# Optimization experiments

Hardware: AMD Instinct MI355X
Metric: run time of the kernel (lower is better)

Reference implementation:

```python
import jax, jax.numpy as jnp
import numpy as np


def _lstm_layer(x, Wih, Whh, b):
    # torch nn.LSTM single layer, batch_first, gates in i,f,g,o order
    B, T, _ = x.shape
    H = Whh.shape[1]
    xg = jnp.einsum('btd,gd->btg', x, Wih) + b  # precompute input gates (B,T,4H)

    def step(carry, g_t):
        h, c = carry
        g = g_t + h @ Whh.T
        i, f, gg, o = jnp.split(g, 4, axis=-1)
        c = jax.nn.sigmoid(f) * c + jax.nn.sigmoid(i) * jnp.tanh(gg)
        h = jax.nn.sigmoid(o) * jnp.tanh(c)
        return (h, c), h

    z = jnp.zeros((B, H), x.dtype)
    _, hs = jax.lax.scan(step, (z, z), jnp.swapaxes(xg, 0, 1))
    return jnp.swapaxes(hs, 0, 1)


def _forward(x, x_lens, word_starts, word_ends, word_lens, tail_frames,
             fW_ih0, fW_hh0, fb0, fW_ih1, fW_hh1, fb1, fW_ih2, fW_hh2, fb2,
             fpW, fpb, wpW, wpb, lnW, lnB, wW_ih, wW_hh, wb, spW, spb):
    B, T, _ = x.shape
    # 3-layer frame LSTM (eval mode: inter-layer dropout disabled)
    h = _lstm_layer(x, fW_ih0, fW_hh0, fb0)
    h = _lstm_layer(h, fW_ih1, fW_hh1, fb1)
    h = _lstm_layer(h, fW_ih2, fW_hh2, fb2)
    # pad_packed_sequence zeros outputs beyond each sequence length
    tmask = (jnp.arange(T)[None, :] < x_lens[:, None]).astype(h.dtype)
    h = h * tmask[..., None]
    y_frame = h @ fpW.T + fpb  # (B,T,srv)

    # ragged per-word tail mean: r_j = mean h[i0:ef], i0 = max(ef-tail, sf)
    W = word_ends.shape[1]
    ef = jnp.minimum(word_ends, x_lens[:, None])
    sf = jnp.maximum(word_starts, 0)
    i0 = jnp.maximum(ef - tail_frames, sf)
    valid = ((jnp.arange(W)[None, :] < word_lens[:, None]) & (word_ends > 0)
             & (ef > sf) & (ef > i0))
    t = jnp.arange(T)
    m = (valid[:, :, None] & (t[None, None, :] >= i0[:, :, None])
         & (t[None, None, :] < ef[:, :, None])).astype(h.dtype)  # (B,W,T)
    cnt = jnp.maximum(m.sum(-1), 1.0)
    reps = jnp.einsum('bwt,bth->bwh', m, h) / cnt[..., None]  # (B,W,FH)

    # word_proj: Linear + LayerNorm + GELU (eval: dropout/noise/word-dropout off)
    r = reps @ wpW.T + wpb
    mu = r.mean(-1, keepdims=True)
    var = ((r - mu) ** 2).mean(-1, keepdims=True)
    r = (r - mu) / jnp.sqrt(var + 1e-5) * lnW + lnB
    r = jax.nn.gelu(r, approximate=False)

    lens = jnp.maximum(word_lens, 1)
    c = _lstm_layer(r, wW_ih, wW_hh, wb)
    wmask = (jnp.arange(W)[None, :] < lens[:, None]).astype(c.dtype)
    c = c * wmask[..., None]  # pad_packed(total_length=W) zeros
    pred_sem = c @ spW.T + spb  # (B,W,srv)
    return y_frame, x_lens, pred_sem


def setup_inputs() -> dict:
    key = jax.random.key(0)
    ks = jax.random.split(key, 24)
    B, T, D, SRV, FH, WR, WH, W = 16, 2000, 80, 512, 512, 256, 256, 100
    x = jax.random.normal(ks[0], (B, T, D), jnp.float32)
    x_lens = jax.random.randint(ks[1], (B,), T // 2, T + 1).at[0].set(T)
    ends = jnp.sort(jax.random.randint(ks[2], (B, W), 1, T + 1), axis=1)
    starts = jnp.concatenate([jnp.zeros((B, 1), ends.dtype), ends[:, :-1]], axis=1)
    word_lens = jax.random.randint(ks[3], (B,), 1, W + 1)

    def u(k, shape, fan):
        s = 1.0 / np.sqrt(fan)
        return jax.random.uniform(k, shape, jnp.float32, -s, s)

    return {
        'x': x, 'x_lens': x_lens, 'word_starts': starts, 'word_ends': ends,
        'word_lens': word_lens, 'tail_frames': 10,
        'fW_ih0': u(ks[4], (4 * FH, D), FH), 'fW_hh0': u(ks[5], (4 * FH, FH), FH), 'fb0': u(ks[6], (4 * FH,), FH),
        'fW_ih1': u(ks[7], (4 * FH, FH), FH), 'fW_hh1': u(ks[8], (4 * FH, FH), FH), 'fb1': u(ks[9], (4 * FH,), FH),
        'fW_ih2': u(ks[10], (4 * FH, FH), FH), 'fW_hh2': u(ks[11], (4 * FH, FH), FH), 'fb2': u(ks[12], (4 * FH,), FH),
        'fpW': u(ks[13], (SRV, FH), FH), 'fpb': u(ks[14], (SRV,), FH),
        'wpW': u(ks[15], (WR, FH), FH), 'wpb': u(ks[16], (WR,), FH),
        'lnW': jnp.ones((WR,), jnp.float32), 'lnB': jnp.zeros((WR,), jnp.float32),
        'wW_ih': u(ks[17], (4 * WH, WR), WH), 'wW_hh': u(ks[18], (4 * WH, WH), WH), 'wb': u(ks[19], (4 * WH,), WH),
        'spW': u(ks[20], (SRV, WH), WH), 'spb': u(ks[21], (SRV,), WH),
    }


def reference(x, x_lens, word_starts, word_ends, word_lens, tail_frames,
              fW_ih0, fW_hh0, fb0, fW_ih1, fW_hh1, fb1, fW_ih2, fW_hh2, fb2,
              fpW, fpb, wpW, wpb, lnW, lnB, wW_ih, wW_hh, wb, spW, spb):
    return _forward(x, x_lens, word_starts, word_ends, word_lens, tail_frames,
                    fW_ih0, fW_hh0, fb0, fW_ih1, fW_hh1, fb1, fW_ih2, fW_hh2, fb2,
                    fpW, fpb, wpW, wpb, lnW, lnB, wW_ih, wW_hh, wb, spW, spb)
```

## Files before the change

kernel.cpp:

```cpp
#include <hip/hip_runtime.h>
#include <math.h>

typedef unsigned short u16;
typedef unsigned int   u32;
typedef unsigned long long u64;
typedef __attribute__((ext_vector_type(8))) short short8;
typedef __attribute__((ext_vector_type(4))) float f32x4;

__device__ __forceinline__ float bf2f(u16 v) { return __uint_as_float(((u32)v) << 16); }
__device__ __forceinline__ u16 f2bf(float f) {
    u32 u = __float_as_uint(f);
    u32 r = (u + 0x7fffu + ((u >> 16) & 1u)) >> 16;
    return (u16)r;
}
__device__ __forceinline__ u32 pk2(float a, float b) {
    return ((u32)f2bf(a)) | (((u32)f2bf(b)) << 16);
}
__device__ __forceinline__ float sigm(float x) { return 1.f / (1.f + __expf(-x)); }
__device__ __forceinline__ f32x4 mfma16(short8 a, short8 b, f32x4 c) {
    return __builtin_amdgcn_mfma_f32_16x16x32_bf16(a, b, c, 0, 0, 0);
}
__device__ __forceinline__ short8 ld8bf(const float* p) {
    short8 r;
#pragma unroll
    for (int j = 0; j < 8; ++j) r[j] = (short)f2bf(p[j]);
    return r;
}
__device__ __forceinline__ short8 ldg16cv(const u16* p) {
    short8 r;
    asm volatile("global_load_dwordx4 %0, %1, off sc0 sc1" : "=v"(r) : "v"(p));
    return r;
}
__device__ __forceinline__ void waitvm() {
    asm volatile("s_waitcnt vmcnt(0)" ::: "memory");
}

#define FLAG_STRIDE 16
#define NPAR 8
#define BIGF (1 << 26)
#define XL_OFF 16384000
#define PS_OFF 16384016

#define WS_FLAGS   0
#define WS_HBUF_F  32768
#define WS_HBUF_W  425984
#define WS_REPS    491520
#define WS_RW      3768320
#define WS_HSEQ    4587520
#define WS_FPWB    6225920

template<int KTIN, bool L0>
__device__ __forceinline__ void frame_body(
    const int layer, const int kwg,
    const float* __restrict__ Wih, const float* __restrict__ Whh, const float* __restrict__ bias,
    const float* __restrict__ x, u16* __restrict__ hbuf, int* __restrict__ flags,
    float* __restrict__ h3out, float* sC, u16* sxpad, u16* AsIn, u16* AsOwn)
{
    const int tid  = threadIdx.x;
    const int lane = tid & 63;
    const int wave = tid >> 6;
    const int n16  = lane & 15;
    const int quad = lane >> 4;
    const int koff = quad * 8;

    if (L0) {
        for (int e = tid; e < 256; e += 128) sxpad[(e >> 4) * 96 + 80 + (e & 15)] = 0;
    }

    const int grow = wave * 1024 + ((n16 >> 3) * 512) + kwg * 8 + (n16 & 7);
    short8 bfr[KTIN + 16];
#pragma unroll
    for (int kt = 0; kt < KTIN; ++kt) {
        short8 v = {0,0,0,0,0,0,0,0};
        const int k = kt * 32 + koff;
        if (L0) { if (k + 8 <= 80) v = ld8bf(Wih + grow * 80 + k); }
        else    { v = ld8bf(Wih + (size_t)grow * 512 + k); }
        bfr[kt] = v;
    }
#pragma unroll
    for (int kt = 0; kt < 16; ++kt)
        bfr[KTIN + kt] = ld8bf(Whh + (size_t)grow * 512 + kt * 32 + koff);

    const int gb = tid & 15;
    const int gp4 = (tid >> 4) & 3;
    const int c0 = kwg * 8 + gp4 * 2;
    const float bI0 = bias[c0],        bI1 = bias[c0 + 1];
    const float bF0 = bias[512 + c0],  bF1 = bias[512 + c0 + 1];
    const float bG0 = bias[1024 + c0], bG1 = bias[1024 + c0 + 1];
    const float bO0 = bias[1536 + c0], bO1 = bias[1536 + c0 + 1];
    float cp0 = 0.f, cp1 = 0.f;

    const int* fP = flags + (layer * 64) * FLAG_STRIDE;
    const int* fO = flags + ((layer + 1) * 64) * FLAG_STRIDE;
    const int* fN = flags + ((layer + 2) * 64) * FLAG_STRIDE;
    int* myflag   = flags + ((layer + 1) * 64 + kwg) * FLAG_STRIDE;
    __syncthreads();

    for (int t = 0; t < 2000; ++t) {
        if (wave == 0) {
            int guard = 0;
            for (;;) {
                const int fp = __hip_atomic_load(fP + lane * FLAG_STRIDE, __ATOMIC_RELAXED, __HIP_MEMORY_SCOPE_AGENT);
                const int fo = __hip_atomic_load(fO + lane * FLAG_STRIDE, __ATOMIC_RELAXED, __HIP_MEMORY_SCOPE_AGENT);
                const int fn = __hip_atomic_load(fN + lane * FLAG_STRIDE, __ATOMIC_RELAXED, __HIP_MEMORY_SCOPE_AGENT);
                if (__all((fp >= t + 1) && (fo >= t) && (fn >= t - 7))) break;
                if (++guard > (1 << 22)) break;
                __builtin_amdgcn_s_sleep(1);
            }
        }
        __syncthreads();

        const u16* hown = hbuf + ((size_t)(layer * NPAR + ((t + 7) & 7))) * 8192;
        short8 rin[8], rown[8];
        float4 xv0, xv1, xv2;
        if (L0) {
            const int e0 = tid, e1 = tid + 128, e2 = tid + 256;
            xv0 = *(const float4*)(x + ((size_t)(e0 / 20) * 2000 + t) * 80 + (e0 % 20) * 4);
            xv1 = *(const float4*)(x + ((size_t)(e1 / 20) * 2000 + t) * 80 + (e1 % 20) * 4);
            if (e2 < 320)
                xv2 = *(const float4*)(x + ((size_t)(e2 / 20) * 2000 + t) * 80 + (e2 % 20) * 4);
        } else {
            const u16* hin = hbuf + ((size_t)((layer - 1) * NPAR + (t & 7))) * 8192;
#pragma unroll
            for (int i = 0; i < 8; ++i) rin[i] = ldg16cv(hin + (tid + 128 * i) * 8);
        }
#pragma unroll
        for (int i = 0; i < 8; ++i) rown[i] = ldg16cv(hown + (tid + 128 * i) * 8);
        waitvm();
        if (L0) {
            const int e0 = tid, e1 = tid + 128, e2 = tid + 256;
            u32* d0 = (u32*)(sxpad + (e0 / 20) * 96 + (e0 % 20) * 4);
            d0[0] = pk2(xv0.x, xv0.y); d0[1] = pk2(xv0.z, xv0.w);
            u32* d1 = (u32*)(sxpad + (e1 / 20) * 96 + (e1 % 20) * 4);
            d1[0] = pk2(xv1.x, xv1.y); d1[1] = pk2(xv1.z, xv1.w);
            if (e2 < 320) {
                u32* d2 = (u32*)(sxpad + (e2 / 20) * 96 + (e2 % 20) * 4);
                d2[0] = pk2(xv2.x, xv2.y); d2[1] = pk2(xv2.z, xv2.w);
            }
        }
#pragma unroll
        for (int i = 0; i < 8; ++i) {
            const int c = tid + 128 * i;
            const int row = c >> 6, col8 = (c & 63) << 3;
            if (!L0) *(short8*)(AsIn + row * 520 + col8) = rin[i];
            *(short8*)(AsOwn + row * 520 + col8) = rown[i];
        }
        __syncthreads();

        f32x4 acc[4] = {{0,0,0,0},{0,0,0,0},{0,0,0,0},{0,0,0,0}};
#pragma unroll
        for (int kt = 0; kt < KTIN; ++kt) {
            short8 a;
            if (L0) a = *(const short8*)(sxpad + n16 * 96 + kt * 32 + koff);
            else    a = *(const short8*)(AsIn + n16 * 520 + kt * 32 + koff);
            acc[kt & 3] = mfma16(a, bfr[kt], acc[kt & 3]);
        }
#pragma unroll
        for (int kt = 0; kt < 16; ++kt) {
            short8 a = *(const short8*)(AsOwn + n16 * 520 + kt * 32 + koff);
            acc[(KTIN + kt) & 3] = mfma16(a, bfr[KTIN + kt], acc[(KTIN + kt) & 3]);
        }
        const f32x4 C = acc[0] + acc[1] + acc[2] + acc[3];
#pragma unroll
        for (int r = 0; r < 4; ++r)
            sC[(wave * 16 + quad * 4 + r) * 17 + n16] = C[r];
        __syncthreads();

        if (tid < 64) {
            const int b = gb, p = gp4;
            float hn0, hn1;
            {
                const float gi = sC[b * 17 + p * 2]            + bI0;
                const float gf = sC[b * 17 + 8 + p * 2]        + bF0;
                const float gg = sC[(16 + b) * 17 + p * 2]     + bG0;
                const float go = sC[(16 + b) * 17 + 8 + p * 2] + bO0;
                const float cn = sigm(gf) * cp0 + sigm(gi) * tanhf(gg);
                hn0 = sigm(go) * tanhf(cn);
                cp0 = cn;
            }
            {
                const float gi = sC[b * 17 + p * 2 + 1]            + bI1;
                const float gf = sC[b * 17 + 8 + p * 2 + 1]        + bF1;
                const float gg = sC[(16 + b) * 17 + p * 2 + 1]     + bG1;
                const float go = sC[(16 + b) * 17 + 8 + p * 2 + 1] + bO1;
                const float cn = sigm(gf) * cp1 + sigm(gi) * tanhf(gg);
                hn1 = sigm(go) * tanhf(cn);
                cp1 = cn;
            }
            const u32 pk = ((u32)f2bf(hn0)) | (((u32)f2bf(hn1)) << 16);
            u32* hdst = (u32*)(hbuf + ((size_t)(layer * NPAR + (t & 7))) * 8192 + b * 512 + kwg * 8 + p * 2);
            __hip_atomic_store(hdst, pk, __ATOMIC_RELAXED, __HIP_MEMORY_SCOPE_AGENT);
            waitvm();
            if (tid == 0)
                __hip_atomic_store(myflag, t + 1, __ATOMIC_RELAXED, __HIP_MEMORY_SCOPE_AGENT);
            if (!L0 && layer == 2) {
                float* hp = h3out + ((size_t)(b * 2000 + t)) * 512 + kwg * 8 + p * 2;
                hp[0] = hn0; hp[1] = hn1;
            }
        }
    }
}

__global__ __launch_bounds__(128, 1) void k_frame_lstm(
    const float* __restrict__ x,
    const float* __restrict__ Wih0, const float* __restrict__ Whh0, const float* __restrict__ b0,
    const float* __restrict__ Wih1, const float* __restrict__ Whh1, const float* __restrict__ b1,
    const float* __restrict__ Wih2, const float* __restrict__ Whh2, const float* __restrict__ b2,
    u16* hbuf, int* flags, float* h3out)
{
    __shared__ __align__(16) u16 sxpad[16 * 96];
    __shared__ __align__(16) u16 AsIn[16 * 520];
    __shared__ __align__(16) u16 AsOwn[16 * 520];
    __shared__ float sC[32 * 17];
    const int wgid = blockIdx.x;
    const int layer = wgid >> 6;
    const int kwg = wgid & 63;
    if (layer == 0)      frame_body<3,  true >(0, kwg, Wih0, Whh0, b0, x, hbuf, flags, h3out, sC, sxpad, AsIn, AsOwn);
    else if (layer == 1) frame_body<16, false>(1, kwg, Wih1, Whh1, b1, x, hbuf, flags, h3out, sC, sxpad, AsIn, AsOwn);
    else                 frame_body<16, false>(2, kwg, Wih2, Whh2, b2, x, hbuf, flags, h3out, sC, sxpad, AsIn, AsOwn);
}

__global__ __launch_bounds__(128, 1) void k_word_lstm(
    const u16* __restrict__ rW, const float* __restrict__ Wih,
    const float* __restrict__ Whh, const float* __restrict__ bias,
    u16* __restrict__ hbufw, int* __restrict__ flags, float* __restrict__ hseq)
{
    __shared__ float sC[32 * 17];
    const int tid = threadIdx.x;
    const int lane = tid & 63;
    const int wave = tid >> 6;
    const int n16 = lane & 15;
    const int quad = lane >> 4;
    const int koff = quad * 8;
    const int kwg = blockIdx.x;

    const int grow = wave * 512 + ((n16 >> 3) * 256) + kwg * 8 + (n16 & 7);
    short8 bfr[16];
#pragma unroll
    for (int kt = 0; kt < 8; ++kt) bfr[kt]     = ld8bf(Wih + (size_t)grow * 256 + kt * 32 + koff);
#pragma unroll
    for (int kt = 0; kt < 8; ++kt) bfr[8 + kt] = ld8bf(Whh + (size_t)grow * 256 + kt * 32 + koff);
    const int gb = tid & 15;
    const int gp4 = (tid >> 4) & 3;
    const int c0 = kwg * 8 + gp4 * 2;
    const float bI0 = bias[c0],       bI1 = bias[c0 + 1];
    const float bF0 = bias[256 + c0], bF1 = bias[256 + c0 + 1];
    const float bG0 = bias[512 + c0], bG1 = bias[512 + c0 + 1];
    const float bO0 = bias[768 + c0], bO1 = bias[768 + c0 + 1];
    float cp0 = 0.f, cp1 = 0.f;
    const int* fO = flags + 320 * FLAG_STRIDE;
    int* myflag   = flags + (320 + kwg) * FLAG_STRIDE;
    __syncthreads();
    const int aoff = n16 * 256 + koff;

    for (int t = 0; t < 100; ++t) {
        if (wave == 0) {
            int guard = 0;
            for (;;) {
                const int fo = (lane < 32)
                    ? __hip_atomic_load(fO + lane * FLAG_STRIDE, __ATOMIC_RELAXED, __HIP_MEMORY_SCOPE_AGENT)
                    : BIGF;
                if (__all(fo >= t)) break;
                if (++guard > (1 << 22)) break;
                __builtin_amdgcn_s_sleep(1);
            }
        }
        __syncthreads();
        const u16* hown = hbufw + ((size_t)((t + 7) & 7)) * 4096;
        short8 ha[8];
#pragma unroll
        for (int kt = 0; kt < 8; ++kt) ha[kt] = ldg16cv(hown + aoff + kt * 32);
        f32x4 acc[4] = {{0,0,0,0},{0,0,0,0},{0,0,0,0},{0,0,0,0}};
#pragma unroll
        for (int kt = 0; kt < 8; ++kt) {
            short8 a = *(const short8*)(rW + ((size_t)(n16 * 100 + t)) * 256 + koff + kt * 32);
            acc[kt & 3] = mfma16(a, bfr[kt], acc[kt & 3]);
        }
        waitvm();
#pragma unroll
        for (int kt = 0; kt < 8; ++kt)
            acc[kt & 3] = mfma16(ha[kt], bfr[8 + kt], acc[kt & 3]);
        const f32x4 C = acc[0] + acc[1] + acc[2] + acc[3];
#pragma unroll
        for (int r = 0; r < 4; ++r) sC[(wave * 16 + quad * 4 + r) * 17 + n16] = C[r];
        __syncthreads();
        if (tid < 64) {
            const int b = gb, p = gp4;
            float hn0, hn1;
            {
                const float gi = sC[b * 17 + p * 2]            + bI0;
                const float gf = sC[b * 17 + 8 + p * 2]        + bF0;
                const float gg = sC[(16 + b) * 17 + p * 2]     + bG0;
                const float go = sC[(16 + b) * 17 + 8 + p * 2] + bO0;
                const float cn = sigm(gf) * cp0 + sigm(gi) * tanhf(gg);
                hn0 = sigm(go) * tanhf(cn);
                cp0 = cn;
            }
            {
                const float gi = sC[b * 17 + p * 2 + 1]            + bI1;
                const float gf = sC[b * 17 + 8 + p * 2 + 1]        + bF1;
                const float gg = sC[(16 + b) * 17 + p * 2 + 1]     + bG1;
                const float go = sC[(16 + b) * 17 + 8 + p * 2 + 1] + bO1;
                const float cn = sigm(gf) * cp1 + sigm(gi) * tanhf(gg);
                hn1 = sigm(go) * tanhf(cn);
                cp1 = cn;
            }
            const u32 pk = ((u32)f2bf(hn0)) | (((u32)f2bf(hn1)) << 16);
            u32* hdst = (u32*)(hbufw + ((size_t)(t & 7)) * 4096 + b * 256 + kwg * 8 + p * 2);
            __hip_atomic_store(hdst, pk, __ATOMIC_RELAXED, __HIP_MEMORY_SCOPE_AGENT);
            waitvm();
            if (tid == 0)
                __hip_atomic_store(myflag, t + 1, __ATOMIC_RELAXED, __HIP_MEMORY_SCOPE_AGENT);
            float* hp = hseq + ((size_t)(b * 100 + t)) * 256 + kwg * 8 + p * 2;
            hp[0] = hn0; hp[1] = hn1;
        }
    }
}

__global__ void k_pool(const float* __restrict__ h3, const int* __restrict__ x_lens,
                       const int* __restrict__ wstarts, const int* __restrict__ wends,
                       const int* __restrict__ wlens, const int* __restrict__ tailp,
                       float* __restrict__ reps)
{
    const int rw = blockIdx.x;
    const int b = rw / 100, w = rw - b * 100;
    const int tid = threadIdx.x;
    const int xl = x_lens[b];
    const int we = wends[rw];
    const int s0 = wstarts[rw];
    const int wl = wlens[b];
    const int tail = tailp[0];
    int ef = we < xl ? we : xl;
    int sf = s0 > 0 ? s0 : 0;
    int i0 = ef - tail; if (i0 < sf) i0 = sf;
    const bool valid = (w < wl) && (we > 0) && (ef > sf) && (ef > i0);
    float a0 = 0.f, a1 = 0.f;
    if (valid) {
        for (int t = i0; t < ef; ++t) {
            const float* hp = h3 + ((size_t)(b * 2000 + t)) * 512;
            a0 += hp[tid];
            a1 += hp[tid + 256];
        }
        const float inv = 1.f / (float)(ef - i0);
        a0 *= inv; a1 *= inv;
    }
    reps[(size_t)rw * 512 + tid] = a0;
    reps[(size_t)rw * 512 + tid + 256] = a1;
}

__global__ __launch_bounds__(256, 2) void k_frame_proj(
    float* __restrict__ y, const int* __restrict__ x_lens,
    const u16* __restrict__ fpWb, const float* __restrict__ fpb)
{
    __shared__ __align__(16) u16 As[16 * 520];
    const int tid = threadIdx.x, lane = tid & 63, wave = tid >> 6;
    const int n16 = lane & 15, quad = lane >> 4, koff = quad * 8;
    const int blk = blockIdx.x;
    const int b = blk / 125;
    const int t0 = (blk - b * 125) * 16;
    const int xl = x_lens[b];
    for (int c = tid; c < 2048; c += 256) {
        const int row = c >> 7;
        const int q = c & 127;
        const int t = t0 + row;
        float4 v = {0.f, 0.f, 0.f, 0.f};
        if (t < xl) v = *(const float4*)(y + ((size_t)(b * 2000 + t)) * 512 + q * 4);
        u32* d = (u32*)(As + row * 520 + q * 4);
        d[0] = pk2(v.x, v.y);
        d[1] = pk2(v.z, v.w);
    }
    __syncthreads();
    const size_t rowbase = (size_t)b * 2000 + t0;
    for (int ct = 0; ct < 8; ++ct) {
        const int col0 = (wave * 8 + ct) * 16;
        f32x4 acc = {0, 0, 0, 0};
#pragma unroll
        for (int kt = 0; kt < 16; ++kt) {
            short8 a = *(const short8*)(As + n16 * 520 + kt * 32 + koff);
            short8 wv = *(const short8*)(fpWb + ((size_t)(col0 + n16)) * 512 + kt * 32 + koff);
            acc = mfma16(a, wv, acc);
        }
        const float bn = fpb[col0 + n16];
#pragma unroll
        for (int r = 0; r < 4; ++r) {
            const int m = quad * 4 + r;
            y[(rowbase + m) * 512 + col0 + n16] = acc[r] + bn;
        }
    }
}

__global__ void k_word_proj(const float* __restrict__ reps, const float* __restrict__ wpW,
                            const float* __restrict__ wpb, const float* __restrict__ lnW,
                            const float* __restrict__ lnB, u16* __restrict__ rW)
{
    __shared__ float sx[512];
    __shared__ float red[512];
    const int tid = threadIdx.x;
    const int row = blockIdx.x;
    for (int k = tid; k < 512; k += 256) sx[k] = reps[(size_t)row * 512 + k];
    __syncthreads();
    float acc = wpb[tid];
    const float4* wr = (const float4*)(wpW + (size_t)tid * 512);
    for (int k4 = 0; k4 < 128; ++k4) {
        const float4 w = wr[k4];
        acc += sx[k4 * 4] * w.x + sx[k4 * 4 + 1] * w.y + sx[k4 * 4 + 2] * w.z + sx[k4 * 4 + 3] * w.w;
    }
    red[tid] = acc; red[256 + tid] = acc * acc;
    __syncthreads();
    for (int s = 128; s > 0; s >>= 1) {
        if (tid < s) { red[tid] += red[tid + s]; red[256 + tid] += red[256 + tid + s]; }
        __syncthreads();
    }
    const float mu = red[0] * (1.f / 256.f);
    float var = red[256] * (1.f / 256.f) - mu * mu;
    if (var < 0.f) var = 0.f;
    const float xn = (acc - mu) * rsqrtf(var + 1e-5f);
    const float yv = xn * lnW[tid] + lnB[tid];
    const float g = 0.5f * yv * (1.0f + erff(yv * 0.70710678118654752f));
    rW[(size_t)row * 256 + tid] = f2bf(g);
}

__global__ void k_pred(const float* __restrict__ hseq, const int* __restrict__ wlens,
                       const float* __restrict__ spW, const float* __restrict__ spb,
                       float* __restrict__ out)
{
    __shared__ float sh[256];
    const int tid = threadIdx.x;
    const int rw = blockIdx.x;
    const int b = rw / 100, w = rw - b * 100;
    int wl = wlens[b]; if (wl < 1) wl = 1;
    const bool valid = (w < wl);
    sh[tid] = valid ? hseq[(size_t)rw * 256 + tid] : 0.f;
    __syncthreads();
    for (int o = tid; o < 512; o += 256) {
        float acc = spb[o];
        const float4* wr = (const float4*)(spW + (size_t)o * 256);
        for (int k4 = 0; k4 < 64; ++k4) {
            const float4 wv = wr[k4];
            acc += sh[k4 * 4] * wv.x + sh[k4 * 4 + 1] * wv.y + sh[k4 * 4 + 2] * wv.z + sh[k4 * 4 + 3] * wv.w;
        }
        out[PS_OFF + (size_t)rw * 512 + o] = acc;
    }
}

__global__ void k_xlens(const int* __restrict__ x_lens, float* __restrict__ out)
{
    const int tid = threadIdx.x;
    if (tid < 16) out[XL_OFF + tid] = (float)x_lens[tid];
}

__global__ void k_cvt(const float* __restrict__ src, u16* __restrict__ dst)
{
    const int e = blockIdx.x * 256 + threadIdx.x;
    const float4 v = *(const float4*)(src + (size_t)e * 4);
    u32* d = (u32*)(dst + (size_t)e * 4);
    d[0] = pk2(v.x, v.y);
    d[1] = pk2(v.z, v.w);
}

__global__ void k_init(u32* __restrict__ p)
{
    const int idx = blockIdx.x * 256 + threadIdx.x;
    u32 v = 0u;
    if (idx < 8192) {
        const int slot = idx >> 4;
        if (slot < 64 || (slot >= 256 && slot < 320)) v = (u32)BIGF;
    }
    p[idx] = v;
}

extern "C" void kernel_launch(void* const* d_in, const int* in_sizes, int n_in,
                              void* d_out, int out_size, void* d_ws, size_t ws_size,
                              hipStream_t stream)
{
    (void)in_sizes; (void)n_in; (void)out_size; (void)ws_size;
    const float* x    = (const float*)d_in[0];
    const int* x_lens = (const int*)d_in[1];
    const int* wstart = (const int*)d_in[2];
    const int* wend   = (const int*)d_in[3];
    const int* wlen   = (const int*)d_in[4];
    const int* tailp  = (const int*)d_in[5];
    const float* Wih0 = (const float*)d_in[6];
    const float* Whh0 = (const float*)d_in[7];
    const float* b0   = (const float*)d_in[8];
    const float* Wih1 = (const float*)d_in[9];
    const float* Whh1 = (const float*)d_in[10];
    const float* b1   = (const float*)d_in[11];
    const float* Wih2 = (const float*)d_in[12];
    const float* Whh2 = (const float*)d_in[13];
    const float* b2   = (const float*)d_in[14];
    const float* fpW  = (const float*)d_in[15];
    const float* fpb  = (const float*)d_in[16];
    const float* wpW  = (const float*)d_in[17];
    const float* wpb  = (const float*)d_in[18];
    const float* lnW  = (const float*)d_in[19];
    const float* lnB  = (const float*)d_in[20];
    const float* wWih = (const float*)d_in[21];
    const float* wWhh = (const float*)d_in[22];
    const float* wb   = (const float*)d_in[23];
    const float* spW  = (const float*)d_in[24];
    const float* spb  = (const float*)d_in[25];

    float* out = (float*)d_out;
    char* ws = (char*)d_ws;
    int* flags  = (int*)(ws + WS_FLAGS);
    u16* hbufF  = (u16*)(ws + WS_HBUF_F);
    u16* hbufW  = (u16*)(ws + WS_HBUF_W);
    float* reps = (float*)(ws + WS_REPS);
    u16* rW     = (u16*)(ws + WS_RW);
    float* hseq = (float*)(ws + WS_HSEQ);
    u16* fpWb   = (u16*)(ws + WS_FPWB);

    k_init<<<480, 256, 0, stream>>>((u32*)d_ws);
    k_cvt<<<256, 256, 0, stream>>>(fpW, fpWb);
    k_frame_lstm<<<192, 128, 0, stream>>>(x, Wih0, Whh0, b0, Wih1, Whh1, b1,
                                          Wih2, Whh2, b2, hbufF, flags, out);
    k_pool<<<1600, 256, 0, stream>>>(out, x_lens, wstart, wend, wlen, tailp, reps);
    k_frame_proj<<<2000, 256, 0, stream>>>(out, x_lens, fpWb, fpb);
    k_word_proj<<<1600, 256, 0, stream>>>(reps, wpW, wpb, lnW, lnB, rW);
    k_word_lstm<<<32, 128, 0, stream>>>(rW, wWih, wWhh, wb, hbufW, flags, hseq);
    k_pred<<<1600, 256, 0, stream>>>(hseq, wlen, spW, spb, out);
    k_xlens<<<1, 64, 0, stream>>>(x_lens, out);
}
```

Baseline: 7.732 ms.

## Fuse frame projection and tail pooling into the layer-2 LSTM recurrence

The layer-2 workgroups now use their otherwise idle second wave to run the frame projection MFMA on the previous step's hidden state and to accumulate per-word tail means, guided by a precomputed frame-to-word map. This removes the separate k_pool and k_frame_proj kernels and the fp32 write and re-read of the full hidden sequence. A new k_wmap kernel builds the map and inverse counts, and a tail pass after the loop handles the last timestep. The map gives each frame a single word, so overlapping word windows are not handled, and the extra work inside the sequential loop could lengthen the critical path.

```diff
diff --git a/kernel.cpp b/kernel.cpp
--- a/kernel.cpp
+++ b/kernel.cpp
@@ -48,13 +48,18 @@
 #define WS_RW      3768320
 #define WS_HSEQ    4587520
 #define WS_FPWB    6225920
-
-template<int KTIN, bool L0>
+#define WS_WMAP    6750208
+#define WS_INV     6878208
+
+template<int KTIN, bool L0, bool PROJ>
 __device__ __forceinline__ void frame_body(
     const int layer, const int kwg,
     const float* __restrict__ Wih, const float* __restrict__ Whh, const float* __restrict__ bias,
     const float* __restrict__ x, u16* __restrict__ hbuf, int* __restrict__ flags,
-    float* __restrict__ h3out, float* sC, u16* sxpad, u16* AsIn, u16* AsOwn)
+    float* __restrict__ yout, const u16* __restrict__ fpWb, const float* __restrict__ fpb,
+    const int* __restrict__ xlens, const int* __restrict__ wmapp,
+    const float* __restrict__ invc, float* __restrict__ reps,
+    float* sC, float* sH, u16* sxpad, u16* AsIn, u16* AsOwn)
 {
     const int tid  = threadIdx.x;
     const int lane = tid & 63;
@@ -89,6 +94,20 @@
     const float bG0 = bias[1024 + c0], bG1 = bias[1024 + c0 + 1];
     const float bO0 = bias[1536 + c0], bO1 = bias[1536 + c0 + 1];
     float cp0 = 0.f, cp1 = 0.f;
+
+    short8 wpr[PROJ ? 16 : 1];
+    int xlr = 0; float fpbr = 0.f;
+    float pa0 = 0.f, pa1 = 0.f; int pw = -1;
+    const int pb = lane >> 2;
+    const int plc = (lane & 3) * 2;
+    if (PROJ) {
+        const int prow = kwg * 8 + (n16 & 7);
+#pragma unroll
+        for (int kt = 0; kt < 16; ++kt)
+            wpr[kt] = *(const short8*)(fpWb + (size_t)prow * 512 + kt * 32 + koff);
+        xlr = xlens[n16];
+        if (n16 < 8) fpbr = fpb[kwg * 8 + n16];
+    }
 
     const int* fP = flags + (layer * 64) * FLAG_STRIDE;
     const int* fO = flags + ((layer + 1) * 64) * FLAG_STRIDE;
@@ -187,15 +206,101 @@
                 hn1 = sigm(go) * tanhf(cn);
                 cp1 = cn;
             }
+            if (PROJ) {
+                sH[(t & 1) * 128 + b * 8 + p * 2] = hn0;
+                sH[(t & 1) * 128 + b * 8 + p * 2 + 1] = hn1;
+            }
             const u32 pk = ((u32)f2bf(hn0)) | (((u32)f2bf(hn1)) << 16);
             u32* hdst = (u32*)(hbuf + ((size_t)(layer * NPAR + (t & 7))) * 8192 + b * 512 + kwg * 8 + p * 2);
             __hip_atomic_store(hdst, pk, __ATOMIC_RELAXED, __HIP_MEMORY_SCOPE_AGENT);
             waitvm();
             if (tid == 0)
                 __hip_atomic_store(myflag, t + 1, __ATOMIC_RELAXED, __HIP_MEMORY_SCOPE_AGENT);
-            if (!L0 && layer == 2) {
-                float* hp = h3out + ((size_t)(b * 2000 + t)) * 512 + kwg * 8 + p * 2;
-                hp[0] = hn0; hp[1] = hn1;
+        } else if (PROJ) {
+            if (t > 0) {
+                const bool rowok = (t - 1) < xlr;
+                const short8 z8 = {0,0,0,0,0,0,0,0};
+                f32x4 pc = {0, 0, 0, 0};
+#pragma unroll
+                for (int kt = 0; kt < 16; ++kt) {
+                    short8 a = rowok ? *(const short8*)(AsOwn + n16 * 520 + kt * 32 + koff) : z8;
+                    pc = mfma16(a, wpr[kt], pc);
+                }
+                if (n16 < 8) {
+#pragma unroll
+                    for (int r = 0; r < 4; ++r)
+                        yout[((size_t)((quad * 4 + r) * 2000 + (t - 1))) * 512 + kwg * 8 + n16] = pc[r] + fpbr;
+                }
+                const int w = wmapp[pb * 2000 + (t - 1)];
+                if (w != pw) {
+                    if (pw >= 0) {
+                        const float iv = invc[pb * 100 + pw];
+                        reps[((size_t)(pb * 100 + pw)) * 512 + kwg * 8 + plc]     = pa0 * iv;
+                        reps[((size_t)(pb * 100 + pw)) * 512 + kwg * 8 + plc + 1] = pa1 * iv;
+                    }
+                    pa0 = pa1 = 0.f; pw = w;
+                }
+                if (w >= 0) {
+                    pa0 += sH[((t - 1) & 1) * 128 + pb * 8 + plc];
+                    pa1 += sH[((t - 1) & 1) * 128 + pb * 8 + plc + 1];
+                }
+            }
+        }
+    }
+
+    if (PROJ) {
+        if (wave == 0) {
+            int guard = 0;
+            for (;;) {
+                const int fo = __hip_atomic_load(fO + lane * FLAG_STRIDE, __ATOMIC_RELAXED, __HIP_MEMORY_SCOPE_AGENT);
+                if (__all(fo >= 2000)) break;
+                if (++guard > (1 << 22)) break;
+                __builtin_amdgcn_s_sleep(1);
+            }
+        }
+        __syncthreads();
+        const u16* hown = hbuf + ((size_t)(layer * NPAR + 7)) * 8192;
+        short8 rown[8];
+#pragma unroll
+        for (int i = 0; i < 8; ++i) rown[i] = ldg16cv(hown + (tid + 128 * i) * 8);
+        waitvm();
+#pragma unroll
+        for (int i = 0; i < 8; ++i) {
+            const int c = tid + 128 * i;
+            *(short8*)(AsOwn + (c >> 6) * 520 + ((c & 63) << 3)) = rown[i];
+        }
+        __syncthreads();
+        if (wave == 1) {
+            const bool rowok = 1999 < xlr;
+            const short8 z8 = {0,0,0,0,0,0,0,0};
+            f32x4 pc = {0, 0, 0, 0};
+#pragma unroll
+            for (int kt = 0; kt < 16; ++kt) {
+                short8 a = rowok ? *(const short8*)(AsOwn + n16 * 520 + kt * 32 + koff) : z8;
+                pc = mfma16(a, wpr[kt], pc);
+            }
+            if (n16 < 8) {
+#pragma unroll
+                for (int r = 0; r < 4; ++r)
+                    yout[((size_t)((quad * 4 + r) * 2000 + 1999)) * 512 + kwg * 8 + n16] = pc[r] + fpbr;
+            }
+            const int w = wmapp[pb * 2000 + 1999];
+            if (w != pw) {
+                if (pw >= 0) {
+                    const float iv = invc[pb * 100 + pw];
+                    reps[((size_t)(pb * 100 + pw)) * 512 + kwg * 8 + plc]     = pa0 * iv;
+                    reps[((size_t)(pb * 100 + pw)) * 512 + kwg * 8 + plc + 1] = pa1 * iv;
+                }
+                pa0 = pa1 = 0.f; pw = w;
+            }
+            if (w >= 0) {
+                pa0 += sH[128 + pb * 8 + plc];
+                pa1 += sH[128 + pb * 8 + plc + 1];
+            }
+            if (pw >= 0) {
+                const float iv = invc[pb * 100 + pw];
+                reps[((size_t)(pb * 100 + pw)) * 512 + kwg * 8 + plc]     = pa0 * iv;
+                reps[((size_t)(pb * 100 + pw)) * 512 + kwg * 8 + plc + 1] = pa1 * iv;
             }
         }
     }
@@ -206,18 +311,50 @@
     const float* __restrict__ Wih0, const float* __restrict__ Whh0, const float* __restrict__ b0,
     const float* __restrict__ Wih1, const float* __restrict__ Whh1, const float* __restrict__ b1,
     const float* __restrict__ Wih2, const float* __restrict__ Whh2, const float* __restrict__ b2,
-    u16* hbuf, int* flags, float* h3out)
+    u16* hbuf, int* flags, float* yout,
+    const u16* __restrict__ fpWb, const float* __restrict__ fpb,
+    const int* __restrict__ xlens, const int* __restrict__ wmapp,
+    const float* __restrict__ invc, float* __restrict__ reps)
 {
     __shared__ __align__(16) u16 sxpad[16 * 96];
     __shared__ __align__(16) u16 AsIn[16 * 520];
     __shared__ __align__(16) u16 AsOwn[16 * 520];
     __shared__ float sC[32 * 17];
+    __shared__ float sH[256];
     const int wgid = blockIdx.x;
     const int layer = wgid >> 6;
     const int kwg = wgid & 63;
-    if (layer == 0)      frame_body<3,  true >(0, kwg, Wih0, Whh0, b0, x, hbuf, flags, h3out, sC, sxpad, AsIn, AsOwn);
-    else if (layer == 1) frame_body<16, false>(1, kwg, Wih1, Whh1, b1, x, hbuf, flags, h3out, sC, sxpad, AsIn, AsOwn);
-    else                 frame_body<16, false>(2, kwg, Wih2, Whh2, b2, x, hbuf, flags, h3out, sC, sxpad, AsIn, AsOwn);
+    if (layer == 0)      frame_body<3,  true,  false>(0, kwg, Wih0, Whh0, b0, x, hbuf, flags, yout, fpWb, fpb, xlens, wmapp, invc, reps, sC, sH, sxpad, AsIn, AsOwn);
+    else if (layer == 1) frame_body<16, false, false>(1, kwg, Wih1, Whh1, b1, x, hbuf, flags, yout, fpWb, fpb, xlens, wmapp, invc, reps, sC, sH, sxpad, AsIn, AsOwn);
+    else                 frame_body<16, false, true >(2, kwg, Wih2, Whh2, b2, x, hbuf, flags, yout, fpWb, fpb, xlens, wmapp, invc, reps, sC, sH, sxpad, AsIn, AsOwn);
+}
+
+__global__ void k_wmap(const int* __restrict__ x_lens, const int* __restrict__ wstarts,
+                       const int* __restrict__ wends, const int* __restrict__ wlens,
+                       const int* __restrict__ tailp, int* __restrict__ wmap,
+                       float* __restrict__ invc, float* __restrict__ out)
+{
+    const int b = blockIdx.x;
+    const int tid = threadIdx.x;
+    for (int t = tid; t < 2000; t += 256) wmap[b * 2000 + t] = -1;
+    if (tid == 0) out[XL_OFF + b] = (float)x_lens[b];
+    __syncthreads();
+    if (tid < 100) {
+        const int w = tid;
+        const int xl = x_lens[b];
+        const int we = wends[b * 100 + w];
+        const int s0 = wstarts[b * 100 + w];
+        const int wl = wlens[b];
+        const int tail = tailp[0];
+        int ef = we < xl ? we : xl;
+        int sf = s0 > 0 ? s0 : 0;
+        int i0 = ef - tail; if (i0 < sf) i0 = sf;
+        const bool valid = (w < wl) && (we > 0) && (ef > sf) && (ef > i0);
+        invc[b * 100 + w] = valid ? 1.f / (float)(ef - i0) : 0.f;
+        if (valid) {
+            for (int t = i0; t < ef; ++t) wmap[b * 2000 + t] = w;
+        }
+    }
 }
 
 __global__ __launch_bounds__(128, 1) void k_word_lstm(
@@ -313,78 +450,6 @@
                 __hip_atomic_store(myflag, t + 1, __ATOMIC_RELAXED, __HIP_MEMORY_SCOPE_AGENT);
             float* hp = hseq + ((size_t)(b * 100 + t)) * 256 + kwg * 8 + p * 2;
             hp[0] = hn0; hp[1] = hn1;
-        }
-    }
-}
-
-__global__ void k_pool(const float* __restrict__ h3, const int* __restrict__ x_lens,
-                       const int* __restrict__ wstarts, const int* __restrict__ wends,
-                       const int* __restrict__ wlens, const int* __restrict__ tailp,
-                       float* __restrict__ reps)
-{
-    const int rw = blockIdx.x;
-    const int b = rw / 100, w = rw - b * 100;
-    const int tid = threadIdx.x;
-    const int xl = x_lens[b];
-    const int we = wends[rw];
-    const int s0 = wstarts[rw];
-    const int wl = wlens[b];
-    const int tail = tailp[0];
-    int ef = we < xl ? we : xl;
-    int sf = s0 > 0 ? s0 : 0;
-    int i0 = ef - tail; if (i0 < sf) i0 = sf;
-    const bool valid = (w < wl) && (we > 0) && (ef > sf) && (ef > i0);
-    float a0 = 0.f, a1 = 0.f;
-    if (valid) {
-        for (int t = i0; t < ef; ++t) {
-            const float* hp = h3 + ((size_t)(b * 2000 + t)) * 512;
-            a0 += hp[tid];
-            a1 += hp[tid + 256];
-        }
-        const float inv = 1.f / (float)(ef - i0);
-        a0 *= inv; a1 *= inv;
-    }
-    reps[(size_t)rw * 512 + tid] = a0;
-    reps[(size_t)rw * 512 + tid + 256] = a1;
-}
-
-__global__ __launch_bounds__(256, 2) void k_frame_proj(
-    float* __restrict__ y, const int* __restrict__ x_lens,
-    const u16* __restrict__ fpWb, const float* __restrict__ fpb)
-{
-    __shared__ __align__(16) u16 As[16 * 520];
-    const int tid = threadIdx.x, lane = tid & 63, wave = tid >> 6;
-    const int n16 = lane & 15, quad = lane >> 4, koff = quad * 8;
-    const int blk = blockIdx.x;
-    const int b = blk / 125;
-    const int t0 = (blk - b * 125) * 16;
-    const int xl = x_lens[b];
-    for (int c = tid; c < 2048; c += 256) {
-        const int row = c >> 7;
-        const int q = c & 127;
-        const int t = t0 + row;
-        float4 v = {0.f, 0.f, 0.f, 0.f};
-        if (t < xl) v = *(const float4*)(y + ((size_t)(b * 2000 + t)) * 512 + q * 4);
-        u32* d = (u32*)(As + row * 520 + q * 4);
-        d[0] = pk2(v.x, v.y);
-        d[1] = pk2(v.z, v.w);
-    }
-    __syncthreads();
-    const size_t rowbase = (size_t)b * 2000 + t0;
-    for (int ct = 0; ct < 8; ++ct) {
-        const int col0 = (wave * 8 + ct) * 16;
-        f32x4 acc = {0, 0, 0, 0};
-#pragma unroll
-        for (int kt = 0; kt < 16; ++kt) {
-            short8 a = *(const short8*)(As + n16 * 520 + kt * 32 + koff);
-            short8 wv = *(const short8*)(fpWb + ((size_t)(col0 + n16)) * 512 + kt * 32 + koff);
-            acc = mfma16(a, wv, acc);
-        }
-        const float bn = fpb[col0 + n16];
-#pragma unroll
-        for (int r = 0; r < 4; ++r) {
-            const int m = quad * 4 + r;
-            y[(rowbase + m) * 512 + col0 + n16] = acc[r] + bn;
         }
     }
 }
@@ -441,12 +506,6 @@
         }
         out[PS_OFF + (size_t)rw * 512 + o] = acc;
     }
-}
-
-__global__ void k_xlens(const int* __restrict__ x_lens, float* __restrict__ out)
-{
-    const int tid = threadIdx.x;
-    if (tid < 16) out[XL_OFF + tid] = (float)x_lens[tid];
 }
 
 __global__ void k_cvt(const float* __restrict__ src, u16* __restrict__ dst)
@@ -510,15 +569,16 @@
     u16* rW     = (u16*)(ws + WS_RW);
     float* hseq = (float*)(ws + WS_HSEQ);
     u16* fpWb   = (u16*)(ws + WS_FPWB);
-
-    k_init<<<480, 256, 0, stream>>>((u32*)d_ws);
+    int* wmap   = (int*)(ws + WS_WMAP);
+    float* invc = (float*)(ws + WS_INV);
+
+    k_init<<<3680, 256, 0, stream>>>((u32*)d_ws);
     k_cvt<<<256, 256, 0, stream>>>(fpW, fpWb);
+    k_wmap<<<16, 256, 0, stream>>>(x_lens, wstart, wend, wlen, tailp, wmap, invc, out);
     k_frame_lstm<<<192, 128, 0, stream>>>(x, Wih0, Whh0, b0, Wih1, Whh1, b1,
-                                          Wih2, Whh2, b2, hbufF, flags, out);
-    k_pool<<<1600, 256, 0, stream>>>(out, x_lens, wstart, wend, wlen, tailp, reps);
-    k_frame_proj<<<2000, 256, 0, stream>>>(out, x_lens, fpWb, fpb);
+                                          Wih2, Whh2, b2, hbufF, flags, out,
+                                          fpWb, fpb, x_lens, wmap, invc, reps);
     k_word_proj<<<1600, 256, 0, stream>>>(reps, wpW, wpb, lnW, lnB, rW);
     k_word_lstm<<<32, 128, 0, stream>>>(rW, wWih, wWhh, wb, hbufW, flags, hseq);
     k_pred<<<1600, 256, 0, stream>>>(hseq, wlen, spW, spb, out);
-    k_xlens<<<1, 64, 0, stream>>>(x_lens, out);
-}
+}
```

Measured after the change: 7.723 ms. No clear change (-0.1%).
